# Optimization experiments

Hardware: AMD Instinct MI355X
Metric: run time of the kernel (lower is better)

Reference implementation:

```python
import jax, jax.numpy as jnp
import numpy as np

EMBED = 256
HEADS = 8
SR = 2
RED = 2


def setup_inputs() -> dict:
    key = jax.random.key(0)
    ks = jax.random.split(key, 12)
    N, B, C = 1024, 64, EMBED
    inp = {
        "query": jax.random.normal(ks[0], (N, B, C), jnp.float32),
        "H": 32,
        "W": 32,
        "key": jax.random.normal(ks[1], (N, B, C), jnp.float32),
        "value": jax.random.normal(ks[2], (N, B, C), jnp.float32),
        # parameters
        "in_proj_weight": jax.random.normal(ks[3], (3 * C, C), jnp.float32) * (1.0 / np.sqrt(C)),
        "in_proj_bias": jnp.zeros((3 * C,), jnp.float32),
        "sr_w": jax.random.normal(ks[4], (C, C, SR, SR), jnp.float32) * np.sqrt(2.0 / (SR * SR * C)),
        "sr_b": jnp.zeros((C,), jnp.float32),
        "norm_g": jnp.ones((C,), jnp.float32),
        "norm_b": jnp.zeros((C,), jnp.float32),
        "out_w": jax.random.normal(ks[5], (C, C), jnp.float32) * (1.0 / np.sqrt(C)),
        "out_b": jnp.zeros((C,), jnp.float32),
        "se_w1": jax.random.normal(ks[6], (C // RED, C), jnp.float32) * 0.02,
        "se_w2": jax.random.normal(ks[7], (C, C // RED), jnp.float32) * 0.02,
    }
    return inp


def _angles(H, W):
    # get_index: a = (pi/2)*(i//W)/H, b = (pi/2)*(i%W)/W for flattened row-major index
    c = np.pi / 2
    idx = jnp.arange(H * W)
    a = c * (idx // W).astype(jnp.float32) / H
    b = c * (idx % W).astype(jnp.float32) / W
    return a, b


def _layernorm(x, g, b, eps=1e-5):
    mu = jnp.mean(x, -1, keepdims=True)
    var = jnp.mean(jnp.square(x - mu), -1, keepdims=True)
    return (x - mu) * jax.lax.rsqrt(var + eps) * g + b


def _abs_clamp(t, lo=1e-4, hi=1e4):
    return jnp.clip(jnp.abs(t), lo, hi) * jnp.sign(t)


def reference(query, H, W, key, value, in_proj_weight, in_proj_bias, sr_w, sr_b,
              norm_g, norm_b, out_w, out_b, se_w1, se_w2):
    N, B, C = query.shape
    h = HEADS
    hd = C // h
    scaling = hd ** (-0.5)

    x = jnp.transpose(query, (1, 0, 2))  # (B, N, C)

    # squeeze-excite gate from query: mean over tokens -> fc1 -> relu -> fc2 -> sigmoid
    se = jnp.mean(x, axis=1)                       # (B, C)
    se = jax.nn.sigmoid(jax.nn.relu(se @ se_w1.T) @ se_w2.T)  # (B, C)

    # spatial reduction conv (kernel=stride=sr_ratio) + layernorm for k/v source
    x_img = jnp.transpose(x, (0, 2, 1)).reshape(B, C, H, W)
    xr = jax.lax.conv_general_dilated(
        x_img, sr_w, window_strides=(SR, SR), padding="VALID",
        dimension_numbers=("NCHW", "OIHW", "NCHW"))
    xr = xr + sr_b[None, :, None, None]
    Hs, Ws = H // SR, W // SR
    Ns = Hs * Ws
    xr = jnp.transpose(xr.reshape(B, C, Ns), (0, 2, 1))  # (B, Ns, C)
    xr = _layernorm(xr, norm_g, norm_b)

    Wq, Wk, Wv = in_proj_weight[:C], in_proj_weight[C:2 * C], in_proj_weight[2 * C:]
    bq, bk, bv = in_proj_bias[:C], in_proj_bias[C:2 * C], in_proj_bias[2 * C:]

    def split_heads(t):  # (B, L, C) -> (B*h, L, hd)
        Bb, L, _ = t.shape
        return jnp.transpose(t.reshape(Bb, L, h, hd), (0, 2, 1, 3)).reshape(Bb * h, L, hd)

    q = split_heads((x @ Wq.T + bq) * scaling)
    k = split_heads(xr @ Wk.T + bk)
    v = split_heads(xr @ Wv.T + bv)

    q = jax.nn.relu(q)
    k = jax.nn.relu(k)

    # cosFormer-2d "sum" reweighting: cos(a_i - a_j) + cos(b_i - b_j)
    a, b = _angles(H, W)       # (N,)
    a2, b2 = _angles(Hs, Ws)   # (Ns,)

    def reweight(t, aa, bb):  # (BH, L, hd), angles (L,) -> (BH, L, 4*hd)
        aa = aa[None, :, None]
        bb = bb[None, :, None]
        return jnp.concatenate(
            [t * jnp.cos(aa), t * jnp.sin(aa), t * jnp.cos(bb), t * jnp.sin(bb)], axis=-1)

    q_ = reweight(q, a, b)     # (BH, N, 4hd)
    k_ = reweight(k, a2, b2)   # (BH, Ns, 4hd)

    # linear attention: never materialize the NxNs matrix
    kv = jnp.einsum("bnd,bnm->bdm", k_, v)             # (BH, 4hd, hd)
    denom = jnp.einsum("bnd,bd->bn", q_, k_.sum(1))    # (BH, N)
    denom = _abs_clamp(denom)
    attn = jnp.einsum("bnd,bdm->bnm", q_, kv) / denom[..., None]  # (BH, N, hd)

    attn = jnp.transpose(attn.reshape(B, h, N, hd), (0, 2, 1, 3)).reshape(B, N, C)
    out = attn @ out_w.T + out_b            # (B, N, C)
    out = out * se[:, None, :]              # SE channel gating
    return jnp.transpose(out, (1, 0, 2))    # (N, B, C)
```

## Files before the change

### kernel.cpp

```cpp
#include <hip/hip_runtime.h>

#define NTOK 1024
#define NB   64
#define CD   256
#define NHEAD 8
#define HDIM 32
#define NS 256
#define NBC 16384

typedef __attribute__((ext_vector_type(8))) short short8v;
typedef __attribute__((ext_vector_type(4))) short short4v;
typedef __attribute__((ext_vector_type(4))) float f32x4;

__device__ __forceinline__ unsigned bfr(float x){
  unsigned u = __float_as_uint(x);
  return (u + 0x7fffu + ((u>>16)&1u)) >> 16;
}
__device__ __forceinline__ void split2(float x, short &h, short &l){
  unsigned hu = bfr(x);
  float hf = __uint_as_float(hu << 16);
  unsigned lu = bfr(x - hf);
  h = (short)hu; l = (short)lu;
}

__global__ __launch_bounds__(256) void k_pre(const float* __restrict__ ipw, const float* __restrict__ ow,
                                             const float* __restrict__ srw,
                                             short* __restrict__ Wih, short* __restrict__ Wil,
                                             short* __restrict__ Woh, short* __restrict__ Wol,
                                             short* __restrict__ Wsh, short* __restrict__ Wsl,
                                             float* __restrict__ t1, float* __restrict__ t2,
                                             const float* __restrict__ query, float* __restrict__ part){
  int bid = blockIdx.x, t = threadIdx.x;
  if (bid < 256){
    int u = bid*256 + t;
    float xs[8];
    short* dh; short* dl; int dof;
    if (u < 24576){
      int n = u >> 5, off = (u & 31)*8;
      const float* s = ipw + n*CD + off;
      #pragma unroll
      for (int i=0;i<8;++i) xs[i] = s[i];
      dh = Wih; dl = Wil; dof = n*CD + off;
    } else if (u < 32768){
      int v = u - 24576;
      int n = v >> 5, off = (v & 31)*8;
      const float* s = ow + n*CD + off;
      #pragma unroll
      for (int i=0;i<8;++i) xs[i] = s[i];
      dh = Woh; dl = Wol; dof = n*CD + off;
    } else {
      int v = u - 32768;
      int n = v >> 7, koff = (v & 127)*8;
      int g = koff >> 8, cin0 = koff & 255;
      #pragma unroll
      for (int i=0;i<8;++i) xs[i] = srw[n*1024 + (cin0+i)*4 + g];
      dh = Wsh; dl = Wsl; dof = n*1024 + koff;
    }
    short8v h, l;
    #pragma unroll
    for (int i=0;i<8;++i){ short a,b; split2(xs[i],a,b); h[i]=a; l[i]=b; }
    *(short8v*)(dh + dof) = h;
    *(short8v*)(dl + dof) = l;
  } else if (bid < 260){
    int n = (bid-256)*256 + t;
    const float c = 1.57079632679489662f;
    float aa = c * (float)(n >> 5) / 32.0f;
    float bb = c * (float)(n & 31) / 32.0f;
    t1[n*4+0]=cosf(aa); t1[n*4+1]=sinf(aa); t1[n*4+2]=cosf(bb); t1[n*4+3]=sinf(bb);
    if (n < 256){
      float a2 = c * (float)(n >> 4) / 16.0f;
      float b2 = c * (float)(n & 15) / 16.0f;
      t2[n*4+0]=cosf(a2); t2[n*4+1]=sinf(a2); t2[n*4+2]=cosf(b2); t2[n*4+3]=sinf(b2);
    }
  } else {
    int vb_ = bid - 260;
    int b = vb_ >> 2, qr = vb_ & 3;
    const float* qp = query + (qr*256)*NBC + b*CD + t;
    float s0=0.f,s1=0.f,s2=0.f,s3=0.f;
    for (int n=0;n<256;n+=4){
      s0 += qp[(n  )*NBC];
      s1 += qp[(n+1)*NBC];
      s2 += qp[(n+2)*NBC];
      s3 += qp[(n+3)*NBC];
    }
    part[vb_*256 + t] = (s0+s1)+(s2+s3);
  }
}

__global__ __launch_bounds__(256) void k_mid(const float* __restrict__ qf,
                                             const short* __restrict__ Wsh, const short* __restrict__ Wsl,
                                             const float* __restrict__ srb, float* __restrict__ xr,
                                             const short* __restrict__ Wih, const short* __restrict__ Wil,
                                             const float* __restrict__ ipb,
                                             short* __restrict__ Qbh, short* __restrict__ Qbl,
                                             const float* __restrict__ part, const float* __restrict__ w1,
                                             const float* __restrict__ w2, float* __restrict__ se){
  __shared__ __align__(16) short smem[16384];
  int bid = blockIdx.x, t = threadIdx.x;
  if (bid < 512){
    short* Ah = smem;
    short* Al = smem + 2048;
    short* Bh = smem + 4096;
    short* Bl = smem + 8192;
    int mblk = bid >> 1, nblk = bid & 1;
    int m0 = mblk*64, n0 = nblk*128;
    int b = mblk >> 2;
    int pos0 = m0 & 255;
    int wave = t>>6, lane = t&63;
    int wm = wave>>1, wn = wave&1;
    int q = lane>>4, r = lane&15;
    int ra = t>>2, pa = (t&3)*8;
    int posA = pos0 + ra, hs = posA>>4, ws2 = posA&15;
    const f32x4 fz = {0.f,0.f,0.f,0.f};
    f32x4 acc[2][4];
    #pragma unroll
    for (int s=0;s<2;++s)
      #pragma unroll
      for (int tt=0;tt<4;++tt) acc[s][tt] = fz;
    for (int kc=0; kc<32; ++kc){
      int g = kc>>3, cin0 = (kc&7)*32;
      int gh = g>>1, gw = g&1;
      int tok = (2*hs+gh)*32 + 2*ws2 + gw;
      const float* src = qf + (size_t)tok*NBC + b*CD + cin0 + pa;
      float4 fa = *(const float4*)src;
      float4 fb = *(const float4*)(src+4);
      float xs[8] = {fa.x,fa.y,fa.z,fa.w,fb.x,fb.y,fb.z,fb.w};
      short8v hh, ll;
      #pragma unroll
      for (int i=0;i<8;++i){ short a0,b0; split2(xs[i],a0,b0); hh[i]=a0; ll[i]=b0; }
      *(short8v*)(Ah + ra*32 + pa) = hh;
      *(short8v*)(Al + ra*32 + pa) = ll;
      int ko = kc*32;
      #pragma unroll
      for (int rep=0; rep<2; ++rep){
        int rr = ra + rep*64;
        int gb = (n0 + rr)*1024 + ko + pa;
        *(short8v*)(Bh + rr*32 + pa) = *(const short8v*)(Wsh + gb);
        *(short8v*)(Bl + rr*32 + pa) = *(const short8v*)(Wsl + gb);
      }
      __syncthreads();
      short8v ah[2], al[2];
      #pragma unroll
      for (int s=0;s<2;++s){
        int row = wm*32 + s*16 + r;
        ah[s] = *(const short8v*)(Ah + row*32 + q*8);
        al[s] = *(const short8v*)(Al + row*32 + q*8);
      }
      #pragma unroll
      for (int tt=0;tt<4;++tt){
        int brow = wn*64 + tt*16 + r;
        short8v bh = *(const short8v*)(Bh + brow*32 + q*8);
        short8v bl = *(const short8v*)(Bl + brow*32 + q*8);
        #pragma unroll
        for (int s=0;s<2;++s){
          acc[s][tt] = __builtin_amdgcn_mfma_f32_16x16x32_bf16(ah[s], bh, acc[s][tt], 0,0,0);
          acc[s][tt] = __builtin_amdgcn_mfma_f32_16x16x32_bf16(ah[s], bl, acc[s][tt], 0,0,0);
          acc[s][tt] = __builtin_amdgcn_mfma_f32_16x16x32_bf16(al[s], bh, acc[s][tt], 0,0,0);
        }
      }
      __syncthreads();
    }
    #pragma unroll
    for (int s=0;s<2;++s){
      #pragma unroll
      for (int tt=0;tt<4;++tt){
        int c = n0 + wn*64 + tt*16 + r;
        float bias = srb[c];
        #pragma unroll
        for (int i=0;i<4;++i){
          int m = m0 + wm*32 + s*16 + q*4 + i;
          xr[m*CD + c] = acc[s][tt][i] + bias;
        }
      }
    }
  } else if (bid < 1536){
    short* Ah = smem;
    short* Al = smem + 4096;
    short* Bh = smem + 8192;
    short* Bl = smem + 12288;
    int qb_ = bid - 512;
    int mblk = qb_ >> 1, nblk = qb_ & 1;
    int m0 = mblk*128, n0 = nblk*128;
    int wave = t>>6, lane = t&63;
    int wm = wave>>1, wn = wave&1;
    int q = lane>>4, r = lane&15;
    int cr = t>>2, cp = (t&3)*8;
    int cpS = (((t&3) ^ ((cr>>1)&3)))*8;
    int sw8 = ((r>>1)&3)*8;
    const f32x4 fz = {0.f,0.f,0.f,0.f};
    f32x4 acc[4][4];
    #pragma unroll
    for (int s=0;s<4;++s)
      #pragma unroll
      for (int tt=0;tt<4;++tt) acc[s][tt] = fz;
    for (int kc=0; kc<8; ++kc){
      int ko = kc*32;
      #pragma unroll
      for (int rep=0; rep<2; ++rep){
        int rr = cr + rep*64;
        int m = m0 + rr;
        const float* src = qf + (size_t)(m & 1023)*NBC + (m >> 10)*CD + ko + cp;
        float4 fa = *(const float4*)src;
        float4 fb = *(const float4*)(src+4);
        float xs[8] = {fa.x,fa.y,fa.z,fa.w,fb.x,fb.y,fb.z,fb.w};
        short8v hh, ll;
        #pragma unroll
        for (int i=0;i<8;++i){ short a0,b0; split2(xs[i],a0,b0); hh[i]=a0; ll[i]=b0; }
        *(short8v*)(Ah + rr*32 + cpS) = hh;
        *(short8v*)(Al + rr*32 + cpS) = ll;
        int gb = (n0 + rr)*CD + ko + cp;
        *(short8v*)(Bh + rr*32 + cpS) = *(const short8v*)(Wih + gb);
        *(short8v*)(Bl + rr*32 + cpS) = *(const short8v*)(Wil + gb);
      }
      __syncthreads();
      short8v ah[4], al[4];
      #pragma unroll
      for (int s=0;s<4;++s){
        int row = wm*64 + s*16 + r;
        ah[s] = *(const short8v*)(Ah + row*32 + ((q*8)^sw8));
        al[s] = *(const short8v*)(Al + row*32 + ((q*8)^sw8));
      }
      #pragma unroll
      for (int tt=0;tt<4;++tt){
        int brow = wn*64 + tt*16 + r;
        short8v bh = *(const short8v*)(Bh + brow*32 + ((q*8)^sw8));
        short8v bl = *(const short8v*)(Bl + brow*32 + ((q*8)^sw8));
        #pragma unroll
        for (int s=0;s<4;++s){
          acc[s][tt] = __builtin_amdgcn_mfma_f32_16x16x32_bf16(ah[s], bh, acc[s][tt], 0,0,0);
          acc[s][tt] = __builtin_amdgcn_mfma_f32_16x16x32_bf16(ah[s], bl, acc[s][tt], 0,0,0);
          acc[s][tt] = __builtin_amdgcn_mfma_f32_16x16x32_bf16(al[s], bh, acc[s][tt], 0,0,0);
        }
      }
      __syncthreads();
    }
    const float sc = 0.17677669529663687f;
    short* T = smem;
    #pragma unroll
    for (int s=0;s<4;++s){
      #pragma unroll
      for (int tt=0;tt<4;++tt){
        int c_loc = wn*64 + tt*16 + r;
        int chunk = c_loc >> 3, cb = c_loc & 7;
        float bias = ipb[n0 + c_loc];
        #pragma unroll
        for (int i=0;i<4;++i){
          int m_loc = wm*64 + s*16 + q*4 + i;
          float val = fmaxf(acc[s][tt][i] + bias, 0.f)*sc;
          unsigned hu = bfr(val);
          T[m_loc*128 + ((chunk ^ (m_loc&7))<<3) + cb] = (short)hu;
          acc[s][tt][i] = val - __uint_as_float(hu<<16);
        }
      }
    }
    __syncthreads();
    {
      int mrl = (lane>>2);
      int ccl = lane&3;
      #pragma unroll
      for (int e=0;e<8;++e){
        int hl = e&3, mg = e>>2;
        int m_loc = wave*32 + mg*16 + mrl;
        int cc16 = hl*4 + ccl;
        short8v v = *(const short8v*)(T + m_loc*128 + ((cc16 ^ (m_loc&7))<<3));
        *(short8v*)(Qbh + ((size_t)((n0>>5)+hl))*2097152 + (size_t)(m0+m_loc)*32 + ccl*8) = v;
      }
    }
    __syncthreads();
    #pragma unroll
    for (int s=0;s<4;++s){
      #pragma unroll
      for (int tt=0;tt<4;++tt){
        int c_loc = wn*64 + tt*16 + r;
        int chunk = c_loc >> 3, cb = c_loc & 7;
        #pragma unroll
        for (int i=0;i<4;++i){
          int m_loc = wm*64 + s*16 + q*4 + i;
          T[m_loc*128 + ((chunk ^ (m_loc&7))<<3) + cb] = (short)bfr(acc[s][tt][i]);
        }
      }
    }
    __syncthreads();
    {
      int mrl = (lane>>2);
      int ccl = lane&3;
      #pragma unroll
      for (int e=0;e<8;++e){
        int hl = e&3, mg = e>>2;
        int m_loc = wave*32 + mg*16 + mrl;
        int cc16 = hl*4 + ccl;
        short8v v = *(const short8v*)(T + m_loc*128 + ((cc16 ^ (m_loc&7))<<3));
        *(short8v*)(Qbl + ((size_t)((n0>>5)+hl))*2097152 + (size_t)(m0+m_loc)*32 + ccl*8) = v;
      }
    }
  } else {
    float* sm = (float*)smem;
    float* s1s = sm + 256;
    int b = bid - 1536;
    float s = (part[(b*4+0)*256+t]+part[(b*4+1)*256+t])+(part[(b*4+2)*256+t]+part[(b*4+3)*256+t]);
    sm[t] = s*(1.0f/1024.0f);
    __syncthreads();
    if (t < 128){
      float a = 0.f;
      const float* wr = w1 + t*256;
      for (int c=0;c<256;c+=4){
        float4 wf = *(const float4*)(wr+c);
        a += sm[c]*wf.x + sm[c+1]*wf.y + sm[c+2]*wf.z + sm[c+3]*wf.w;
      }
      s1s[t] = fmaxf(a, 0.f);
    }
    __syncthreads();
    float a = 0.f;
    const float* wr2 = w2 + t*128;
    for (int c=0;c<128;c+=4){
      float4 wf = *(const float4*)(wr2+c);
      a += s1s[c]*wf.x + s1s[c+1]*wf.y + s1s[c+2]*wf.z + s1s[c+3]*wf.w;
    }
    se[b*256+t] = 1.0f/(1.0f+expf(-a));
  }
}

__global__ __launch_bounds__(256) void k_kvproj(const float* __restrict__ xr, const float* __restrict__ lng,
                                                const float* __restrict__ lnb,
                                                const short* __restrict__ Wkh, const short* __restrict__ Wkl,
                                                const float* __restrict__ ipb, float* __restrict__ kb,
                                                float* __restrict__ vb){
  __shared__ __align__(16) short Ah[128*32];
  __shared__ __align__(16) short Al[128*32];
  __shared__ __align__(16) short Bh[128*32];
  __shared__ __align__(16) short Bl[128*32];
  __shared__ float mu_s[128];
  __shared__ float inv_s[128];
  int mblk = blockIdx.x >> 2, nblk = blockIdx.x & 3;
  int m0 = mblk*128, n0 = nblk*128;
  int t = threadIdx.x, wave = t>>6, lane = t&63;
  int wm = wave>>1, wn = wave&1;
  int q = lane>>4, r = lane&15;
  int cr = t>>2, cp = (t&3)*8;
  for (int rr8=0; rr8<32; ++rr8){
    int rr = rr8*4 + wave;
    float4 v = ((const float4*)(xr + (size_t)(m0+rr)*CD))[lane];
    float s = (v.x+v.y)+(v.z+v.w);
    #pragma unroll
    for (int off=1; off<64; off<<=1) s += __shfl_xor(s, off, 64);
    float mu = s * (1.0f/256.0f);
    float dx=v.x-mu, dy=v.y-mu, dz=v.z-mu, dw=v.w-mu;
    float s2 = (dx*dx+dy*dy)+(dz*dz+dw*dw);
    #pragma unroll
    for (int off=1; off<64; off<<=1) s2 += __shfl_xor(s2, off, 64);
    float inv = 1.0f / sqrtf(s2*(1.0f/256.0f) + 1e-5f);
    if (lane==0){ mu_s[rr]=mu; inv_s[rr]=inv; }
  }
  __syncthreads();
  const f32x4 fz = {0.f,0.f,0.f,0.f};
  f32x4 acc[4][4];
  #pragma unroll
  for (int s=0;s<4;++s)
    #pragma unroll
    for (int tt=0;tt<4;++tt) acc[s][tt] = fz;
  for (int kc=0; kc<8; ++kc){
    int ko = kc*32;
    #pragma unroll
    for (int rep=0; rep<2; ++rep){
      int rr = cr + rep*64;
      const float* src = xr + (size_t)(m0+rr)*CD + ko + cp;
      float4 fa = *(const float4*)src;
      float4 fb = *(const float4*)(src+4);
      float xs[8] = {fa.x,fa.y,fa.z,fa.w,fb.x,fb.y,fb.z,fb.w};
      float4 g0 = *(const float4*)(lng + ko + cp);
      float4 g1 = *(const float4*)(lng + ko + cp + 4);
      float4 b0 = *(const float4*)(lnb + ko + cp);
      float4 b1 = *(const float4*)(lnb + ko + cp + 4);
      float gv[8] = {g0.x,g0.y,g0.z,g0.w,g1.x,g1.y,g1.z,g1.w};
      float bv[8] = {b0.x,b0.y,b0.z,b0.w,b1.x,b1.y,b1.z,b1.w};
      float mu = mu_s[rr], inv = inv_s[rr];
      short8v hh, ll;
      #pragma unroll
      for (int i=0;i<8;++i){
        short a0,bq; split2(((xs[i]-mu)*inv)*gv[i] + bv[i], a0,bq);
        hh[i]=a0; ll[i]=bq;
      }
      *(short8v*)(Ah + rr*32 + cp) = hh;
      *(short8v*)(Al + rr*32 + cp) = ll;
      int gb = (n0 + rr)*CD + ko + cp;
      *(short8v*)(Bh + rr*32 + cp) = *(const short8v*)(Wkh + gb);
      *(short8v*)(Bl + rr*32 + cp) = *(const short8v*)(Wkl + gb);
    }
    __syncthreads();
    short8v ah[4], al[4];
    #pragma unroll
    for (int s=0;s<4;++s){
      int row = wm*64 + s*16 + r;
      ah[s] = *(const short8v*)(Ah + row*32 + q*8);
      al[s] = *(const short8v*)(Al + row*32 + q*8);
    }
    #pragma unroll
    for (int tt=0;tt<4;++tt){
      int brow = wn*64 + tt*16 + r;
      short8v bh = *(const short8v*)(Bh + brow*32 + q*8);
      short8v bl = *(const short8v*)(Bl + brow*32 + q*8);
      #pragma unroll
      for (int s=0;s<4;++s){
        acc[s][tt] = __builtin_amdgcn_mfma_f32_16x16x32_bf16(ah[s], bh, acc[s][tt], 0,0,0);
        acc[s][tt] = __builtin_amdgcn_mfma_f32_16x16x32_bf16(ah[s], bl, acc[s][tt], 0,0,0);
        acc[s][tt] = __builtin_amdgcn_mfma_f32_16x16x32_bf16(al[s], bh, acc[s][tt], 0,0,0);
      }
    }
    __syncthreads();
  }
  #pragma unroll
  for (int s=0;s<4;++s){
    #pragma unroll
    for (int tt=0;tt<4;++tt){
      int c = n0 + wn*64 + tt*16 + r;
      float bias = ipb[256 + c];
      #pragma unroll
      for (int i=0;i<4;++i){
        int m = m0 + wm*64 + s*16 + q*4 + i;
        float v = acc[s][tt][i] + bias;
        if (c < 256) kb[m*CD + c] = fmaxf(v, 0.f);
        else         vb[m*CD + (c-256)] = v;
      }
    }
  }
}

__global__ __launch_bounds__(256) void k_kvattn(const float* __restrict__ kb, const float* __restrict__ vbuf,
                                                const float* __restrict__ t2,
                                                const short* __restrict__ Qbh, const short* __restrict__ Qbl,
                                                const float* __restrict__ t1,
                                                short* __restrict__ Ath, short* __restrict__ Atl){
  __shared__ __align__(16) short Bh[144*32];
  __shared__ __align__(16) short Bl[144*32];
  __shared__ __align__(16) short Ah[256*32];
  __shared__ __align__(16) short Al[256*32];
  int bh = blockIdx.x, b = bh>>3, h = bh&7;
  int t = threadIdx.x, lane = t&63, wave = t>>6;
  int q = lane>>4, r = lane&15;
  {
    int jq = t >> 5, m = t & 31;
    float acc[4][4];
    #pragma unroll
    for (int p=0;p<4;++p){ acc[p][0]=0.f; acc[p][1]=0.f; acc[p][2]=0.f; acc[p][3]=0.f; }
    const float* kbase = kb + h*HDIM + jq*4;
    const float* vbase = vbuf + h*HDIM + m;
    for (int n=0;n<256;++n){
      int ro = (b*NS + n)*CD;
      float4 k4 = *(const float4*)(kbase + ro);
      float vv = vbase[ro];
      float4 tt = *(const float4*)(t2 + n*4);
      float tv[4] = {tt.x, tt.y, tt.z, tt.w};
      float kk[4] = {k4.x, k4.y, k4.z, k4.w};
      #pragma unroll
      for (int p=0;p<4;++p){
        float tp = tv[p]*vv;
        #pragma unroll
        for (int jj=0;jj<4;++jj) acc[p][jj] += tp*kk[jj];
      }
    }
    #pragma unroll
    for (int p=0;p<4;++p){
      short4v h4, l4;
      #pragma unroll
      for (int jj=0;jj<4;++jj){ short a,bq; split2(acc[p][jj],a,bq); h4[jj]=a; l4[jj]=bq; }
      *(short4v*)(Bh + (p*32+m)*32 + jq*4) = h4;
      *(short4v*)(Bl + (p*32+m)*32 + jq*4) = l4;
    }
    if (t < 128){
      int p = t >> 5, j = t & 31;
      float s=0.f;
      const float* kp = kb + h*HDIM + j;
      for (int n=0;n<256;++n) s += t2[n*4+p]*kp[(b*NS+n)*CD];
      short a,bq; split2(s,a,bq);
      Bh[(128+p)*32 + j] = a;
      Bl[(128+p)*32 + j] = bq;
    } else {
      int idx = t - 128;
      #pragma unroll
      for (int ii=0;ii<3;++ii){
        Bh[4224 + idx*3 + ii] = 0;
        Bl[4224 + idx*3 + ii] = 0;
      }
    }
  }
  __syncthreads();
  short8v bf_h[9], bf_l[9];
  #pragma unroll
  for (int nt=0; nt<9; ++nt){
    int row = nt*16 + r;
    bf_h[nt] = *(const short8v*)(Bh + row*32 + q*8);
    bf_l[nt] = *(const short8v*)(Bl + row*32 + q*8);
  }
  const short* qh_base = Qbh + ((size_t)h*65536 + (size_t)b*1024)*32;
  const short* ql_base = Qbl + ((size_t)h*65536 + (size_t)b*1024)*32;
  const f32x4 fz = {0.f,0.f,0.f,0.f};
  for (int u=0; u<4; ++u){
    __syncthreads();
    {
      const short8v* sh = (const short8v*)(qh_base + (u*256 + t)*32);
      const short8v* sl = (const short8v*)(ql_base + (u*256 + t)*32);
      short8v* dh = (short8v*)(Ah + t*32);
      short8v* dl = (short8v*)(Al + t*32);
      #pragma unroll
      for (int i=0;i<4;++i){ dh[i]=sh[i]; dl[i]=sl[i]; }
    }
    __syncthreads();
    #pragma unroll
    for (int mi=0; mi<4; ++mi){
      int mt = wave*4 + mi;
      short8v ah = *(const short8v*)(Ah + (mt*16 + r)*32 + q*8);
      short8v al = *(const short8v*)(Al + (mt*16 + r)*32 + q*8);
      f32x4 acc[9];
      #pragma unroll
      for (int nt=0;nt<9;++nt) acc[nt]=fz;
      #pragma unroll
      for (int nt=0;nt<9;++nt){
        acc[nt] = __builtin_amdgcn_mfma_f32_16x16x32_bf16(ah, bf_h[nt], acc[nt],0,0,0);
        acc[nt] = __builtin_amdgcn_mfma_f32_16x16x32_bf16(ah, bf_l[nt], acc[nt],0,0,0);
        acc[nt] = __builtin_amdgcn_mfma_f32_16x16x32_bf16(al, bf_h[nt], acc[nt],0,0,0);
      }
      int nbase = u*256 + mt*16 + q*4;
      int src = lane & 48;
      #pragma unroll
      for (int i=0;i<4;++i){
        int n = nbase + i;
        float4 tv = *(const float4*)(t1 + n*4);
        float dp0 = __shfl(acc[8][i], src+0, 64);
        float dp1 = __shfl(acc[8][i], src+1, 64);
        float dp2 = __shfl(acc[8][i], src+2, 64);
        float dp3 = __shfl(acc[8][i], src+3, 64);
        float den = tv.x*dp0 + tv.y*dp1 + tv.z*dp2 + tv.w*dp3;
        float a0 = tv.x*acc[0][i] + tv.y*acc[2][i] + tv.z*acc[4][i] + tv.w*acc[6][i];
        float a1 = tv.x*acc[1][i] + tv.y*acc[3][i] + tv.z*acc[5][i] + tv.w*acc[7][i];
        float sgn = (den>0.f) ? 1.f : ((den<0.f)? -1.f : 0.f);
        float ad = fminf(fmaxf(fabsf(den), 1e-4f), 1e4f);
        float inv = (den != 0.f) ? 1.0f/(ad*sgn) : 0.f;
        float o0 = a0*inv, o1 = a1*inv;
        int mrow = b*NTOK + n;
        short h0,l0,h1,l1;
        split2(o0,h0,l0); split2(o1,h1,l1);
        Ath[mrow*CD + h*HDIM + r]      = h0;
        Atl[mrow*CD + h*HDIM + r]      = l0;
        Ath[mrow*CD + h*HDIM + 16 + r] = h1;
        Atl[mrow*CD + h*HDIM + 16 + r] = l1;
      }
    }
  }
}

__global__ __launch_bounds__(256) void k_outproj(const short* __restrict__ Ath, const short* __restrict__ Atl,
                                                 const short* __restrict__ Woh, const short* __restrict__ Wol,
                                                 const float* __restrict__ obv, const float* __restrict__ se,
                                                 float* __restrict__ dout){
  __shared__ __align__(16) short Ah[128*32];
  __shared__ __align__(16) short Al[128*32];
  __shared__ __align__(16) short Bh[128*32];
  __shared__ __align__(16) short Bl[128*32];
  int mblk = blockIdx.x >> 1, nblk = blockIdx.x & 1;
  int m0 = mblk*128, n0 = nblk*128;
  int t = threadIdx.x, wave = t>>6, lane = t&63;
  int wm = wave>>1, wn = wave&1;
  int q = lane>>4, r = lane&15;
  int cr = t>>2, cp = (t&3)*8;
  const f32x4 fz = {0.f,0.f,0.f,0.f};
  f32x4 acc[4][4];
  #pragma unroll
  for (int s=0;s<4;++s)
    #pragma unroll
    for (int tt=0;tt<4;++tt) acc[s][tt] = fz;
  for (int kc=0; kc<8; ++kc){
    int ko = kc*32;
    #pragma unroll
    for (int rep=0; rep<2; ++rep){
      int rr = cr + rep*64;
      int ga = (m0 + rr)*CD + ko + cp;
      *(short8v*)(Ah + rr*32 + cp) = *(const short8v*)(Ath + ga);
      *(short8v*)(Al + rr*32 + cp) = *(const short8v*)(Atl + ga);
      int gb = (n0 + rr)*CD + ko + cp;
      *(short8v*)(Bh + rr*32 + cp) = *(const short8v*)(Woh + gb);
      *(short8v*)(Bl + rr*32 + cp) = *(const short8v*)(Wol + gb);
    }
    __syncthreads();
    short8v ah[4], al[4];
    #pragma unroll
    for (int s=0;s<4;++s){
      int row = wm*64 + s*16 + r;
      ah[s] = *(const short8v*)(Ah + row*32 + q*8);
      al[s] = *(const short8v*)(Al + row*32 + q*8);
    }
    #pragma unroll
    for (int tt=0;tt<4;++tt){
      int brow = wn*64 + tt*16 + r;
      short8v bh = *(const short8v*)(Bh + brow*32 + q*8);
      short8v bl = *(const short8v*)(Bl + brow*32 + q*8);
      #pragma unroll
      for (int s=0;s<4;++s){
        acc[s][tt] = __builtin_amdgcn_mfma_f32_16x16x32_bf16(ah[s], bh, acc[s][tt], 0,0,0);
        acc[s][tt] = __builtin_amdgcn_mfma_f32_16x16x32_bf16(ah[s], bl, acc[s][tt], 0,0,0);
        acc[s][tt] = __builtin_amdgcn_mfma_f32_16x16x32_bf16(al[s], bh, acc[s][tt], 0,0,0);
      }
    }
    __syncthreads();
  }
  #pragma unroll
  for (int s=0;s<4;++s){
    #pragma unroll
    for (int tt=0;tt<4;++tt){
      int c = n0 + wn*64 + tt*16 + r;
      float bias = obv[c];
      #pragma unroll
      for (int i=0;i<4;++i){
        int m = m0 + wm*64 + s*16 + q*4 + i;
        int bb = m >> 10, ntok = m & 1023;
        float sev = se[bb*CD + c];
        dout[(ntok*NB + bb)*CD + c] = (acc[s][tt][i] + bias)*sev;
      }
    }
  }
}

extern "C" void kernel_launch(void* const* d_in, const int* in_sizes, int n_in,
                              void* d_out, int out_size, void* d_ws, size_t ws_size,
                              hipStream_t stream) {
  const float* query = (const float*)d_in[0];
  const float* ipw = (const float*)d_in[5];
  const float* ipb = (const float*)d_in[6];
  const float* srw = (const float*)d_in[7];
  const float* srb = (const float*)d_in[8];
  const float* ng  = (const float*)d_in[9];
  const float* nbb = (const float*)d_in[10];
  const float* ow  = (const float*)d_in[11];
  const float* obv = (const float*)d_in[12];
  const float* sw1 = (const float*)d_in[13];
  const float* sw2 = (const float*)d_in[14];
  float* dout = (float*)d_out;
  float* ws = (float*)d_ws;

  short* Qbh  = (short*)ws;
  short* Qbl  = (short*)(ws + 8388608);
  float* R1   = ws + 16777216;
  float* kb   = R1;
  float* vb   = R1 + 4194304;
  short* Ath  = (short*)(R1 + 8388608);
  short* Atl  = (short*)(ws + 33554432);
  float* xr   = ws + 33554432;
  float* part = ws + 44302336;
  float* se   = ws + 44367872;
  float* t1   = ws + 44384256;
  float* t2   = ws + 44388352;
  short* Wih  = (short*)(ws + 44389376);
  short* Wil  = (short*)(ws + 44487680);
  short* Woh  = (short*)(ws + 44585984);
  short* Wol  = (short*)(ws + 44618752);
  short* Wsh  = (short*)(ws + 44651520);
  short* Wsl  = (short*)(ws + 44782592);

  k_pre   <<<516,  256,0,stream>>>(ipw, ow, srw, Wih, Wil, Woh, Wol, Wsh, Wsl, t1, t2, query, part);
  k_mid   <<<1600, 256,0,stream>>>(query, Wsh, Wsl, srb, xr, Wih, Wil, ipb, Qbh, Qbl, part, sw1, sw2, se);
  k_kvproj<<<512,  256,0,stream>>>(xr, ng, nbb, Wih + 256*CD, Wil + 256*CD, ipb, kb, vb);
  k_kvattn<<<512,  256,0,stream>>>(kb, vb, t2, Qbh, Qbl, t1, Ath, Atl);
  k_outproj<<<1024,256,0,stream>>>(Ath, Atl, Woh, Wol, obv, se, dout);
}
```

Measured before the change: 447.9 us.

## Fuse five stage kernels into one persistent cooperative kernel with grid syncs

```diff
diff --git a/kernel.cpp b/kernel.cpp
--- a/kernel.cpp
+++ b/kernel.cpp
@@ -1,4 +1,7 @@
 #include <hip/hip_runtime.h>
+#include <hip/hip_cooperative_groups.h>
+
+namespace cg = cooperative_groups;
 
 #define NTOK 1024
 #define NB   64
@@ -23,14 +26,14 @@
   h = (short)hu; l = (short)lu;
 }
 
-__global__ __launch_bounds__(256) void k_pre(const float* __restrict__ ipw, const float* __restrict__ ow,
-                                             const float* __restrict__ srw,
-                                             short* __restrict__ Wih, short* __restrict__ Wil,
-                                             short* __restrict__ Woh, short* __restrict__ Wol,
-                                             short* __restrict__ Wsh, short* __restrict__ Wsl,
-                                             float* __restrict__ t1, float* __restrict__ t2,
-                                             const float* __restrict__ query, float* __restrict__ part){
-  int bid = blockIdx.x, t = threadIdx.x;
+
+static __device__ __forceinline__ void body_pre(int bid, int t,
+    const float* __restrict__ ipw, const float* __restrict__ ow, const float* __restrict__ srw,
+    short* __restrict__ Wih, short* __restrict__ Wil, short* __restrict__ Woh, short* __restrict__ Wol,
+    short* __restrict__ Wsh, short* __restrict__ Wsl,
+    float* __restrict__ t1, float* __restrict__ t2,
+    const float* __restrict__ query, float* __restrict__ part)
+{
   if (bid < 256){
     int u = bid*256 + t;
     float xs[8];
@@ -87,16 +90,16 @@
   }
 }
 
-__global__ __launch_bounds__(256) void k_mid(const float* __restrict__ qf,
-                                             const short* __restrict__ Wsh, const short* __restrict__ Wsl,
-                                             const float* __restrict__ srb, float* __restrict__ xr,
-                                             const short* __restrict__ Wih, const short* __restrict__ Wil,
-                                             const float* __restrict__ ipb,
-                                             short* __restrict__ Qbh, short* __restrict__ Qbl,
-                                             const float* __restrict__ part, const float* __restrict__ w1,
-                                             const float* __restrict__ w2, float* __restrict__ se){
-  __shared__ __align__(16) short smem[16384];
-  int bid = blockIdx.x, t = threadIdx.x;
+static __device__ __forceinline__ void body_mid(int bid, int t, short* smem,
+    const float* __restrict__ qf,
+    const short* __restrict__ Wsh, const short* __restrict__ Wsl,
+    const float* __restrict__ srb, float* __restrict__ xr,
+    const short* __restrict__ Wih, const short* __restrict__ Wil,
+    const float* __restrict__ ipb,
+    short* __restrict__ Qbh, short* __restrict__ Qbl,
+    const float* __restrict__ part, const float* __restrict__ w1,
+    const float* __restrict__ w2, float* __restrict__ se)
+{
   if (bid < 512){
     short* Ah = smem;
     short* Al = smem + 2048;
@@ -320,20 +323,20 @@
   }
 }
 
-__global__ __launch_bounds__(256) void k_kvproj(const float* __restrict__ xr, const float* __restrict__ lng,
-                                                const float* __restrict__ lnb,
-                                                const short* __restrict__ Wkh, const short* __restrict__ Wkl,
-                                                const float* __restrict__ ipb, float* __restrict__ kb,
-                                                float* __restrict__ vb){
-  __shared__ __align__(16) short Ah[128*32];
-  __shared__ __align__(16) short Al[128*32];
-  __shared__ __align__(16) short Bh[128*32];
-  __shared__ __align__(16) short Bl[128*32];
-  __shared__ float mu_s[128];
-  __shared__ float inv_s[128];
-  int mblk = blockIdx.x >> 2, nblk = blockIdx.x & 3;
+static __device__ __forceinline__ void body_kvproj(int bid, int t, short* smem, float* stats,
+    const float* __restrict__ xr, const float* __restrict__ lng, const float* __restrict__ lnb,
+    const short* __restrict__ Wkh, const short* __restrict__ Wkl,
+    const float* __restrict__ ipb, float* __restrict__ kb, float* __restrict__ vb)
+{
+  short* Ah = smem;
+  short* Al = smem + 4096;
+  short* Bh = smem + 8192;
+  short* Bl = smem + 12288;
+  float* mu_s = stats;
+  float* inv_s = stats + 128;
+  int mblk = bid >> 2, nblk = bid & 3;
   int m0 = mblk*128, n0 = nblk*128;
-  int t = threadIdx.x, wave = t>>6, lane = t&63;
+  int wave = t>>6, lane = t&63;
   int wm = wave>>1, wn = wave&1;
   int q = lane>>4, r = lane&15;
   int cr = t>>2, cp = (t&3)*8;
@@ -425,17 +428,17 @@
   }
 }
 
-__global__ __launch_bounds__(256) void k_kvattn(const float* __restrict__ kb, const float* __restrict__ vbuf,
-                                                const float* __restrict__ t2,
-                                                const short* __restrict__ Qbh, const short* __restrict__ Qbl,
-                                                const float* __restrict__ t1,
-                                                short* __restrict__ Ath, short* __restrict__ Atl){
-  __shared__ __align__(16) short Bh[144*32];
-  __shared__ __align__(16) short Bl[144*32];
-  __shared__ __align__(16) short Ah[256*32];
-  __shared__ __align__(16) short Al[256*32];
-  int bh = blockIdx.x, b = bh>>3, h = bh&7;
-  int t = threadIdx.x, lane = t&63, wave = t>>6;
+static __device__ __forceinline__ void body_kvattn(int bid, int t, short* sm,
+    const float* __restrict__ kb, const float* __restrict__ vbuf, const float* __restrict__ t2,
+    const short* __restrict__ Qbh, const short* __restrict__ Qbl, const float* __restrict__ t1,
+    short* __restrict__ Ath, short* __restrict__ Atl)
+{
+  short* Bh = sm;
+  short* Bl = sm + 4608;
+  short* Ah = sm + 9216;
+  short* Al = sm + 11264;
+  int bh = bid, b = bh>>3, h = bh&7;
+  int lane = t&63, wave = t>>6;
   int q = lane>>4, r = lane&15;
   {
     int jq = t >> 5, m = t & 31;
@@ -494,71 +497,65 @@
   const short* qh_base = Qbh + ((size_t)h*65536 + (size_t)b*1024)*32;
   const short* ql_base = Qbl + ((size_t)h*65536 + (size_t)b*1024)*32;
   const f32x4 fz = {0.f,0.f,0.f,0.f};
-  for (int u=0; u<4; ++u){
+  for (int u=0; u<16; ++u){
     __syncthreads();
     {
-      const short8v* sh = (const short8v*)(qh_base + (u*256 + t)*32);
-      const short8v* sl = (const short8v*)(ql_base + (u*256 + t)*32);
-      short8v* dh = (short8v*)(Ah + t*32);
-      short8v* dl = (short8v*)(Al + t*32);
-      #pragma unroll
-      for (int i=0;i<4;++i){ dh[i]=sh[i]; dl[i]=sl[i]; }
-    }
-    __syncthreads();
-    #pragma unroll
-    for (int mi=0; mi<4; ++mi){
-      int mt = wave*4 + mi;
-      short8v ah = *(const short8v*)(Ah + (mt*16 + r)*32 + q*8);
-      short8v al = *(const short8v*)(Al + (mt*16 + r)*32 + q*8);
-      f32x4 acc[9];
-      #pragma unroll
-      for (int nt=0;nt<9;++nt) acc[nt]=fz;
-      #pragma unroll
-      for (int nt=0;nt<9;++nt){
-        acc[nt] = __builtin_amdgcn_mfma_f32_16x16x32_bf16(ah, bf_h[nt], acc[nt],0,0,0);
-        acc[nt] = __builtin_amdgcn_mfma_f32_16x16x32_bf16(ah, bf_l[nt], acc[nt],0,0,0);
-        acc[nt] = __builtin_amdgcn_mfma_f32_16x16x32_bf16(al, bf_h[nt], acc[nt],0,0,0);
-      }
-      int nbase = u*256 + mt*16 + q*4;
-      int src = lane & 48;
-      #pragma unroll
-      for (int i=0;i<4;++i){
-        int n = nbase + i;
-        float4 tv = *(const float4*)(t1 + n*4);
-        float dp0 = __shfl(acc[8][i], src+0, 64);
-        float dp1 = __shfl(acc[8][i], src+1, 64);
-        float dp2 = __shfl(acc[8][i], src+2, 64);
-        float dp3 = __shfl(acc[8][i], src+3, 64);
-        float den = tv.x*dp0 + tv.y*dp1 + tv.z*dp2 + tv.w*dp3;
-        float a0 = tv.x*acc[0][i] + tv.y*acc[2][i] + tv.z*acc[4][i] + tv.w*acc[6][i];
-        float a1 = tv.x*acc[1][i] + tv.y*acc[3][i] + tv.z*acc[5][i] + tv.w*acc[7][i];
-        float sgn = (den>0.f) ? 1.f : ((den<0.f)? -1.f : 0.f);
-        float ad = fminf(fmaxf(fabsf(den), 1e-4f), 1e4f);
-        float inv = (den != 0.f) ? 1.0f/(ad*sgn) : 0.f;
-        float o0 = a0*inv, o1 = a1*inv;
-        int mrow = b*NTOK + n;
-        short h0,l0,h1,l1;
-        split2(o0,h0,l0); split2(o1,h1,l1);
-        Ath[mrow*CD + h*HDIM + r]      = h0;
-        Atl[mrow*CD + h*HDIM + r]      = l0;
-        Ath[mrow*CD + h*HDIM + 16 + r] = h1;
-        Atl[mrow*CD + h*HDIM + 16 + r] = l1;
-      }
-    }
-  }
-}
-
-__global__ __launch_bounds__(256) void k_outproj(const short* __restrict__ Ath, const short* __restrict__ Atl,
-                                                 const short* __restrict__ Woh, const short* __restrict__ Wol,
-                                                 const float* __restrict__ obv, const float* __restrict__ se,
-                                                 float* __restrict__ dout){
-  __shared__ __align__(16) short Ah[128*32];
-  __shared__ __align__(16) short Al[128*32];
-  __shared__ __align__(16) short Bh[128*32];
-  __shared__ __align__(16) short Bl[128*32];
-  int mblk = blockIdx.x >> 1, nblk = blockIdx.x & 1;
+      int row = t>>2, seg = (t&3)*8;
+      *(short8v*)(Ah + row*32 + seg) = *(const short8v*)(qh_base + (size_t)(u*64 + row)*32 + seg);
+      *(short8v*)(Al + row*32 + seg) = *(const short8v*)(ql_base + (size_t)(u*64 + row)*32 + seg);
+    }
+    __syncthreads();
+    short8v ah = *(const short8v*)(Ah + (wave*16 + r)*32 + q*8);
+    short8v al = *(const short8v*)(Al + (wave*16 + r)*32 + q*8);
+    f32x4 acc[9];
+    #pragma unroll
+    for (int nt=0;nt<9;++nt) acc[nt]=fz;
+    #pragma unroll
+    for (int nt=0;nt<9;++nt){
+      acc[nt] = __builtin_amdgcn_mfma_f32_16x16x32_bf16(ah, bf_h[nt], acc[nt],0,0,0);
+      acc[nt] = __builtin_amdgcn_mfma_f32_16x16x32_bf16(ah, bf_l[nt], acc[nt],0,0,0);
+      acc[nt] = __builtin_amdgcn_mfma_f32_16x16x32_bf16(al, bf_h[nt], acc[nt],0,0,0);
+    }
+    int nbase = u*64 + wave*16 + q*4;
+    int src = lane & 48;
+    #pragma unroll
+    for (int i=0;i<4;++i){
+      int n = nbase + i;
+      float4 tv = *(const float4*)(t1 + n*4);
+      float dp0 = __shfl(acc[8][i], src+0, 64);
+      float dp1 = __shfl(acc[8][i], src+1, 64);
+      float dp2 = __shfl(acc[8][i], src+2, 64);
+      float dp3 = __shfl(acc[8][i], src+3, 64);
+      float den = tv.x*dp0 + tv.y*dp1 + tv.z*dp2 + tv.w*dp3;
+      float a0 = tv.x*acc[0][i] + tv.y*acc[2][i] + tv.z*acc[4][i] + tv.w*acc[6][i];
+      float a1 = tv.x*acc[1][i] + tv.y*acc[3][i] + tv.z*acc[5][i] + tv.w*acc[7][i];
+      float sgn = (den>0.f) ? 1.f : ((den<0.f)? -1.f : 0.f);
+      float ad = fminf(fmaxf(fabsf(den), 1e-4f), 1e4f);
+      float inv = (den != 0.f) ? 1.0f/(ad*sgn) : 0.f;
+      float o0 = a0*inv, o1 = a1*inv;
+      int mrow = b*NTOK + n;
+      short h0,l0,h1,l1;
+      split2(o0,h0,l0); split2(o1,h1,l1);
+      Ath[mrow*CD + h*HDIM + r]      = h0;
+      Atl[mrow*CD + h*HDIM + r]      = l0;
+      Ath[mrow*CD + h*HDIM + 16 + r] = h1;
+      Atl[mrow*CD + h*HDIM + 16 + r] = l1;
+    }
+  }
+}
+
+static __device__ __forceinline__ void body_outproj(int bid, int t, short* smem,
+    const short* __restrict__ Ath, const short* __restrict__ Atl,
+    const short* __restrict__ Woh, const short* __restrict__ Wol,
+    const float* __restrict__ obv, const float* __restrict__ se, float* __restrict__ dout)
+{
+  short* Ah = smem;
+  short* Al = smem + 4096;
+  short* Bh = smem + 8192;
+  short* Bl = smem + 12288;
+  int mblk = bid >> 1, nblk = bid & 1;
   int m0 = mblk*128, n0 = nblk*128;
-  int t = threadIdx.x, wave = t>>6, lane = t&63;
+  int wave = t>>6, lane = t&63;
   int wm = wave>>1, wn = wave&1;
   int q = lane>>4, r = lane&15;
   int cr = t>>2, cp = (t&3)*8;
@@ -617,6 +614,96 @@
       }
     }
   }
+}
+
+__global__ __launch_bounds__(256, 3) void k_all(
+    const float* __restrict__ query, const float* __restrict__ ipw, const float* __restrict__ ipb,
+    const float* __restrict__ srw, const float* __restrict__ srb,
+    const float* __restrict__ ng, const float* __restrict__ nbb,
+    const float* __restrict__ ow, const float* __restrict__ obv,
+    const float* __restrict__ sw1, const float* __restrict__ sw2,
+    float* __restrict__ dout, float* __restrict__ ws)
+{
+  __shared__ __align__(16) char arena[34816];
+  short* smem = (short*)arena;
+  float* stats = (float*)(arena + 32768);
+  short* Qbh = (short*)ws;
+  short* Qbl = (short*)(ws + 8388608);
+  float* kb  = ws + 16777216;
+  float* vb  = ws + 20971520;
+  short* Ath = (short*)(ws + 25165824);
+  float* xr  = ws + 33554432;
+  short* Atl = (short*)(ws + 33554432);
+  float* part= ws + 44302336;
+  float* se  = ws + 44367872;
+  float* t1  = ws + 44384256;
+  float* t2  = ws + 44388352;
+  short* Wih = (short*)(ws + 44389376);
+  short* Wil = (short*)(ws + 44487680);
+  short* Woh = (short*)(ws + 44585984);
+  short* Wol = (short*)(ws + 44618752);
+  short* Wsh = (short*)(ws + 44651520);
+  short* Wsl = (short*)(ws + 44782592);
+  int t = threadIdx.x;
+  cg::grid_group grid = cg::this_grid();
+
+  for (int bid = blockIdx.x; bid < 516; bid += gridDim.x)
+    body_pre(bid, t, ipw, ow, srw, Wih, Wil, Woh, Wol, Wsh, Wsl, t1, t2, query, part);
+  grid.sync();
+  for (int bid = blockIdx.x; bid < 1600; bid += gridDim.x){
+    __syncthreads();
+    body_mid(bid, t, smem, query, Wsh, Wsl, srb, xr, Wih, Wil, ipb, Qbh, Qbl, part, sw1, sw2, se);
+  }
+  grid.sync();
+  for (int bid = blockIdx.x; bid < 512; bid += gridDim.x){
+    __syncthreads();
+    body_kvproj(bid, t, smem, stats, xr, ng, nbb, Wih + 256*CD, Wil + 256*CD, ipb, kb, vb);
+  }
+  grid.sync();
+  for (int bid = blockIdx.x; bid < 512; bid += gridDim.x){
+    __syncthreads();
+    body_kvattn(bid, t, smem, kb, vb, t2, Qbh, Qbl, t1, Ath, Atl);
+  }
+  grid.sync();
+  for (int bid = blockIdx.x; bid < 1024; bid += gridDim.x){
+    __syncthreads();
+    body_outproj(bid, t, smem, Ath, Atl, Woh, Wol, obv, se, dout);
+  }
+}
+
+__global__ __launch_bounds__(256) void k_pre(const float* __restrict__ ipw, const float* __restrict__ ow,
+    const float* __restrict__ srw, short* __restrict__ Wih, short* __restrict__ Wil,
+    short* __restrict__ Woh, short* __restrict__ Wol, short* __restrict__ Wsh, short* __restrict__ Wsl,
+    float* __restrict__ t1, float* __restrict__ t2, const float* __restrict__ query, float* __restrict__ part){
+  body_pre(blockIdx.x, threadIdx.x, ipw, ow, srw, Wih, Wil, Woh, Wol, Wsh, Wsl, t1, t2, query, part);
+}
+__global__ __launch_bounds__(256) void k_mid(const float* __restrict__ qf,
+    const short* __restrict__ Wsh, const short* __restrict__ Wsl, const float* __restrict__ srb,
+    float* __restrict__ xr, const short* __restrict__ Wih, const short* __restrict__ Wil,
+    const float* __restrict__ ipb, short* __restrict__ Qbh, short* __restrict__ Qbl,
+    const float* __restrict__ part, const float* __restrict__ w1, const float* __restrict__ w2,
+    float* __restrict__ se){
+  __shared__ __align__(16) short smem[16384];
+  body_mid(blockIdx.x, threadIdx.x, smem, qf, Wsh, Wsl, srb, xr, Wih, Wil, ipb, Qbh, Qbl, part, w1, w2, se);
+}
+__global__ __launch_bounds__(256) void k_kvproj(const float* __restrict__ xr, const float* __restrict__ lng,
+    const float* __restrict__ lnb, const short* __restrict__ Wkh, const short* __restrict__ Wkl,
+    const float* __restrict__ ipb, float* __restrict__ kb, float* __restrict__ vb){
+  __shared__ __align__(16) short smem[16384];
+  __shared__ float stats[256];
+  body_kvproj(blockIdx.x, threadIdx.x, smem, stats, xr, lng, lnb, Wkh, Wkl, ipb, kb, vb);
+}
+__global__ __launch_bounds__(256) void k_kvattn(const float* __restrict__ kb, const float* __restrict__ vbuf,
+    const float* __restrict__ t2, const short* __restrict__ Qbh, const short* __restrict__ Qbl,
+    const float* __restrict__ t1, short* __restrict__ Ath, short* __restrict__ Atl){
+  __shared__ __align__(16) short sm[13312];
+  body_kvattn(blockIdx.x, threadIdx.x, sm, kb, vbuf, t2, Qbh, Qbl, t1, Ath, Atl);
+}
+__global__ __launch_bounds__(256) void k_outproj(const short* __restrict__ Ath, const short* __restrict__ Atl,
+    const short* __restrict__ Woh, const short* __restrict__ Wol, const float* __restrict__ obv,
+    const float* __restrict__ se, float* __restrict__ dout){
+  __shared__ __align__(16) short smem[16384];
+  body_outproj(blockIdx.x, threadIdx.x, smem, Ath, Atl, Woh, Wol, obv, se, dout);
 }
 
 extern "C" void kernel_launch(void* const* d_in, const int* in_sizes, int n_in,
@@ -634,30 +721,35 @@
   const float* sw1 = (const float*)d_in[13];
   const float* sw2 = (const float*)d_in[14];
   float* dout = (float*)d_out;
-  float* ws = (float*)d_ws;
-
-  short* Qbh  = (short*)ws;
-  short* Qbl  = (short*)(ws + 8388608);
-  float* R1   = ws + 16777216;
-  float* kb   = R1;
-  float* vb   = R1 + 4194304;
-  short* Ath  = (short*)(R1 + 8388608);
-  short* Atl  = (short*)(ws + 33554432);
-  float* xr   = ws + 33554432;
-  float* part = ws + 44302336;
-  float* se   = ws + 44367872;
-  float* t1   = ws + 44384256;
-  float* t2   = ws + 44388352;
-  short* Wih  = (short*)(ws + 44389376);
-  short* Wil  = (short*)(ws + 44487680);
-  short* Woh  = (short*)(ws + 44585984);
-  short* Wol  = (short*)(ws + 44618752);
-  short* Wsh  = (short*)(ws + 44651520);
-  short* Wsl  = (short*)(ws + 44782592);
-
-  k_pre   <<<516,  256,0,stream>>>(ipw, ow, srw, Wih, Wil, Woh, Wol, Wsh, Wsl, t1, t2, query, part);
-  k_mid   <<<1600, 256,0,stream>>>(query, Wsh, Wsl, srb, xr, Wih, Wil, ipb, Qbh, Qbl, part, sw1, sw2, se);
-  k_kvproj<<<512,  256,0,stream>>>(xr, ng, nbb, Wih + 256*CD, Wil + 256*CD, ipb, kb, vb);
-  k_kvattn<<<512,  256,0,stream>>>(kb, vb, t2, Qbh, Qbl, t1, Ath, Atl);
-  k_outproj<<<1024,256,0,stream>>>(Ath, Atl, Woh, Wol, obv, se, dout);
-}
+  float* wsp = (float*)d_ws;
+
+  void* args[] = { (void*)&query, (void*)&ipw, (void*)&ipb, (void*)&srw, (void*)&srb,
+                   (void*)&ng, (void*)&nbb, (void*)&ow, (void*)&obv, (void*)&sw1,
+                   (void*)&sw2, (void*)&dout, (void*)&wsp };
+  hipError_t e = hipLaunchCooperativeKernel((const void*)k_all, dim3(768), dim3(256), args, 0, stream);
+  if (e != hipSuccess){
+    float* ws = wsp;
+    short* Qbh = (short*)ws;
+    short* Qbl = (short*)(ws + 8388608);
+    float* kb  = ws + 16777216;
+    float* vb  = ws + 20971520;
+    short* Ath = (short*)(ws + 25165824);
+    float* xr  = ws + 33554432;
+    short* Atl = (short*)(ws + 33554432);
+    float* part= ws + 44302336;
+    float* se  = ws + 44367872;
+    float* t1  = ws + 44384256;
+    float* t2  = ws + 44388352;
+    short* Wih = (short*)(ws + 44389376);
+    short* Wil = (short*)(ws + 44487680);
+    short* Woh = (short*)(ws + 44585984);
+    short* Wol = (short*)(ws + 44618752);
+    short* Wsh = (short*)(ws + 44651520);
+    short* Wsl = (short*)(ws + 44782592);
+    k_pre   <<<516,  256,0,stream>>>(ipw, ow, srw, Wih, Wil, Woh, Wol, Wsh, Wsl, t1, t2, query, part);
+    k_mid   <<<1600, 256,0,stream>>>(query, Wsh, Wsl, srb, xr, Wih, Wil, ipb, Qbh, Qbl, part, sw1, sw2, se);
+    k_kvproj<<<512,  256,0,stream>>>(xr, ng, nbb, Wih + 256*CD, Wil + 256*CD, ipb, kb, vb);
+    k_kvattn<<<512,  256,0,stream>>>(kb, vb, t2, Qbh, Qbl, t1, Ath, Atl);
+    k_outproj<<<1024,256,0,stream>>>(Ath, Atl, Woh, Wol, obv, se, dout);
+  }
+}
```

Result: slower. 913.2 us (+103.9%).
